# Kernel tuning notes

Hardware: AMD Instinct MI355X
Metric: run time of the kernel (lower is better)

Reference implementation:

```python
import jax, jax.numpy as jnp
import numpy as np

NEG = -1e30  # finite stand-in for -inf (keeps grads NaN-free)

T, B, V, L = 1024, 64, 128, 256


def setup_inputs() -> dict:
    key = jax.random.key(0)
    k1, k2 = jax.random.split(key)
    acts = jax.random.normal(k1, (T, B, V), dtype=jnp.float32)
    # flat concatenated labels, values in [1, V) (0 is the blank)
    labels = jax.random.randint(k2, (B * L,), 1, V, dtype=jnp.int32)
    act_lens = jnp.full((B,), T, dtype=jnp.int32)
    label_lens = jnp.full((B,), L, dtype=jnp.int32)
    return {"acts": acts, "labels": labels, "act_lens": act_lens, "label_lens": label_lens}


def _ctc_costs(acts, labels, act_lens, label_lens):
    # warp-ctc takes raw activations and applies softmax internally
    Tt, Bb, Vv = acts.shape
    Ll = labels.shape[0] // Bb
    blank = 0
    lab = labels.reshape(Bb, Ll)
    S = 2 * Ll + 1
    # extended label seq: blank, l1, blank, l2, ..., blank  -> (B, S)
    ext = jnp.full((Bb, S), blank, dtype=labels.dtype).at[:, 1::2].set(lab)
    # skip transition allowed where ext[s] != blank and ext[s] != ext[s-2]
    allow = jnp.concatenate(
        [jnp.zeros((Bb, 2), dtype=bool), (ext[:, 2:] != blank) & (ext[:, 2:] != ext[:, :-2])],
        axis=1,
    )
    log_probs = jax.nn.log_softmax(acts, axis=-1)  # (T, B, V)
    # emission log-probs along the extended label sequence: (T, B, S)
    emit_all = jnp.take_along_axis(log_probs, jnp.broadcast_to(ext[None], (Tt, Bb, S)), axis=2)

    alpha0 = (
        jnp.full((Bb, S), NEG, dtype=acts.dtype)
        .at[:, 0].set(emit_all[0, :, 0])
        .at[:, 1].set(emit_all[0, :, 1])
    )

    def step(alpha, xs):
        emit, t = xs  # emit: (B, S)
        p1 = jnp.pad(alpha[:, :-1], ((0, 0), (1, 0)), constant_values=NEG)
        p2 = jnp.pad(alpha[:, :-2], ((0, 0), (2, 0)), constant_values=NEG)
        p2 = jnp.where(allow, p2, NEG)
        m = jnp.maximum(jnp.maximum(alpha, p1), p2)
        new = m + jnp.log(jnp.exp(alpha - m) + jnp.exp(p1 - m) + jnp.exp(p2 - m)) + emit
        # freeze rows whose act_len is exhausted
        alpha = jnp.where((t < act_lens)[:, None], new, alpha)
        return alpha, None

    alphaT, _ = jax.lax.scan(step, alpha0, (emit_all[1:], jnp.arange(1, Tt)))
    end = (2 * label_lens).astype(jnp.int32)  # last blank position per example
    a_end = jnp.take_along_axis(alphaT, end[:, None], axis=1)[:, 0]
    a_end1 = jnp.take_along_axis(alphaT, (end - 1)[:, None], axis=1)[:, 0]
    return -jnp.logaddexp(a_end, a_end1)  # per-example negative log-likelihood


def reference(acts, labels, act_lens, label_lens):
    costs = _ctc_costs(acts, labels, act_lens, label_lens)
    return jnp.sum(costs)  # reduce=True, no size/length averaging
```

## Files before the change

kernel.cpp:

```cpp
#include <hip/hip_runtime.h>
#include <hip/hip_fp16.h>
#include <math.h>


#define L2E 1.4426950408889634f
#define LN2 0.6931471805599453f

constexpr int T   = 1024;
constexpr int B   = 64;
constexpr int V   = 128;
constexpr int L   = 256;
constexpr int RW  = 256;
constexpr int TP  = T + 32;

typedef float v2f __attribute__((ext_vector_type(2)));

__device__ __forceinline__ v2f pk_add(v2f a, v2f b) {
  v2f d; asm("v_pk_add_f32 %0, %1, %2" : "=v"(d) : "v"(a), "v"(b)); return d;
}
__device__ __forceinline__ v2f pk_mul(v2f a, v2f b) {
  v2f d; asm("v_pk_mul_f32 %0, %1, %2" : "=v"(d) : "v"(a), "v"(b)); return d;
}
__device__ __forceinline__ v2f pk_fma(v2f a, v2f b, v2f c) {
  v2f d; asm("v_pk_fma_f32 %0, %1, %2, %3" : "=v"(d) : "v"(a), "v"(b), "v"(c));
  return d;
}

template <int CTRL>
__device__ __forceinline__ float fdpp0(float x) {
  return __int_as_float(__builtin_amdgcn_update_dpp(
      0, __float_as_int(x), CTRL, 0xf, 0xf, true));
}
template <int CTRL>
__device__ __forceinline__ float fdppk(float x) {
  return __int_as_float(__builtin_amdgcn_update_dpp(
      __float_as_int(x), __float_as_int(x), CTRL, 0xf, 0xf, false));
}

__device__ __forceinline__ float wave_bcast63(float x) {
  return __int_as_float(__builtin_amdgcn_readlane(__float_as_int(x), 63));
}

__device__ __forceinline__ float wave_max(float x) {
  x = fmaxf(x, fdppk<0x111>(x));
  x = fmaxf(x, fdppk<0x112>(x));
  x = fmaxf(x, fdppk<0x114>(x));
  x = fmaxf(x, fdppk<0x118>(x));
  x = fmaxf(x, fdppk<0x142>(x));
  x = fmaxf(x, fdppk<0x143>(x));
  return wave_bcast63(x);
}
__device__ __forceinline__ float wave_sum_nn(float x) {
  x += fdpp0<0x111>(x);
  x += fdpp0<0x112>(x);
  x += fdpp0<0x114>(x);
  x += fdpp0<0x118>(x);
  x += fdpp0<0x142>(x);
  x += fdpp0<0x143>(x);
  return wave_bcast63(x);
}

__device__ __forceinline__ float h2f(uint bits) {
  return __half2float(__ushort_as_half((ushort)bits));
}

__global__ __launch_bounds__(512) void ctc_probs_kernel(
    const float* __restrict__ acts,
    const int* __restrict__ labels,
    ushort* __restrict__ P,
    float* __restrict__ Pbk) {
  const int w    = threadIdx.x >> 6;
  const int lane = threadIdx.x & 63;
  const int t    = blockIdx.x * 8 + w;
  const int b    = blockIdx.y;
  ushort* prow = P + ((size_t)b * TP + t) * RW;

  if (t >= T) {
    uint2 z; z.x = 0u; z.y = 0u;
    *(uint2*)(prow + 4 * lane) = z;
    if (lane == 0) {
      v2f zp; zp.x = 0.f; zp.y = 0.f;
      *(v2f*)(Pbk + ((size_t)b * TP + t) * 2) = zp;
    }
    return;
  }

  const float* row = acts + ((size_t)t * B + b) * V;
  const float2 v2 = *(const float2*)(row + 2 * lane);
  const float e0 = exp2f(fmaf(v2.x, L2E, -32.0f));
  const float e1 = exp2f(fmaf(v2.y, L2E, -32.0f));
  const float sm = wave_sum_nn(e0 + e1);
  const float r  = __builtin_amdgcn_rcpf(sm);

  const auto pk = __builtin_amdgcn_cvt_pkrtz(e0 * r, e1 * r);
  uint hp;
  __builtin_memcpy(&hp, &pk, 4);

  const int4 lv = *(const int4*)(labels + (size_t)b * L + 4 * lane);
  const uint g0 = (uint)__builtin_amdgcn_ds_bpermute((lv.x & ~1) * 2, (int)hp);
  const uint g1 = (uint)__builtin_amdgcn_ds_bpermute((lv.y & ~1) * 2, (int)hp);
  const uint g2 = (uint)__builtin_amdgcn_ds_bpermute((lv.z & ~1) * 2, (int)hp);
  const uint g3 = (uint)__builtin_amdgcn_ds_bpermute((lv.w & ~1) * 2, (int)hp);
  const uint h0 = (g0 >> ((lv.x & 1) << 4)) & 0xffffu;
  const uint h1 = (g1 >> ((lv.y & 1) << 4)) & 0xffffu;
  const uint h2 = (g2 >> ((lv.z & 1) << 4));
  const uint h3 = (g3 >> ((lv.w & 1) << 4));
  uint2 o;
  o.x = h0 | (h2 << 16);
  o.y = h1 | (h3 << 16);
  *(uint2*)(prow + 4 * lane) = o;
  if (lane == 0) {
    const float pb = e0 * r;
    v2f bp; bp.x = pb; bp.y = pb;
    *(v2f*)(Pbk + ((size_t)b * TP + t) * 2) = bp;
  }
}

__global__ __launch_bounds__(64) void ctc_dp_kernel(
    const ushort* __restrict__ P,
    const float* __restrict__ Pbk,
    const int* __restrict__ labels,
    const int* __restrict__ act_lens,
    const int* __restrict__ label_lens,
    float* __restrict__ out) {
  const int b    = blockIdx.x;
  const int lane = threadIdx.x;
  const ushort* __restrict__ Pb = P + (size_t)b * TP * RW;
  const float*  __restrict__ Bk = Pbk + (size_t)b * TP * 2;

  const int4 lv   = *(const int4*)(labels + (size_t)b * L + 4 * lane);
  const int prevw = __builtin_amdgcn_update_dpp(0, lv.w, 0x138, 0xf, 0xf, true);
  const float f0 = (lane > 0 && lv.x != 0 && lv.x != prevw) ? 1.f : 0.f;
  const float f1 = (lv.y != 0 && lv.y != lv.x) ? 1.f : 0.f;
  const float f2 = (lv.z != 0 && lv.z != lv.y) ? 1.f : 0.f;
  const float f3 = (lv.w != 0 && lv.w != lv.z) ? 1.f : 0.f;
  v2f F02; F02.x = f0; F02.y = f2;
  v2f F13; F13.x = f1; F13.y = f3;

  const int AL = act_lens[b];

  v2f P0, P1, P2, P3;
  P0.x=0.f; P0.y=0.f; P1.x=0.f; P1.y=0.f;
  P2.x=0.f; P2.y=0.f; P3.x=0.f; P3.y=0.f;
  float a8 = 0.f;
  {
    const uint2 u0 = *(const uint2*)(Pb + 4 * lane);
    const v2f bk0  = *(const v2f*)(Bk);
    const float eb0 = bk0.x;
    const float e00 = h2f(u0.x);
    if (lane == 0) { P0.x = eb0; P1.x = e00; }
  }
  int iacc = 0;
  float pend = 1.0f;

  auto step = [&](uint2 u, v2f eb) {
    const float pc = fdpp0<0x138>(P3.y);
    v2f Q; Q.x = pc; Q.y = P3.x;
    v2f E02, E13;
    E02.x = h2f(u.x); E02.y = h2f(u.x >> 16);
    E13.x = h2f(u.y); E13.y = h2f(u.y >> 16);
    const v2f S0 = pk_add(P0, Q);
    const v2f S1 = pk_add(P1, P0);
    const v2f S2 = pk_add(P2, P1);
    const v2f S3 = pk_add(P3, P2);
    const v2f T1 = pk_fma(F02, Q,  S1);
    const v2f T3 = pk_fma(F13, P1, S3);
    const float s8 = a8 + P3.y;
    P0 = pk_mul(S0, eb);
    P2 = pk_mul(S2, eb);
    P1 = pk_mul(T1, E02);
    P3 = pk_mul(T3, E13);
    a8 = s8 * eb.x;
  };

  auto measure = [&]() {
    float m = fmaxf(fmaxf(fmaxf(P0.x, P0.y), fmaxf(P1.x, P1.y)),
                    fmaxf(fmaxf(P2.x, P2.y), fmaxf(P3.x, P3.y)));
    m = fmaxf(m, a8);
    pend = wave_max(m);
  };
  auto apply = [&]() {
    const uint mb = __float_as_uint(pend);
    int e = (int)((mb >> 23) & 0xffu); if (e < 1) e = 1;
    const float r = __uint_as_float((uint)(254 - e) << 23);
    iacc += (e - 127);
    v2f rr; rr.x = r; rr.y = r;
    P0 = pk_mul(P0, rr); P1 = pk_mul(P1, rr);
    P2 = pk_mul(P2, rr); P3 = pk_mul(P3, rr);
    a8 *= r;
  };

  uint2 ev[16];
  v2f   ebk[16];
  #pragma unroll
  for (int k = 0; k < 16; ++k) {
    ev[k]  = *(const uint2*)(Pb + (size_t)(1 + k) * RW + 4 * lane);
    ebk[k] = *(const v2f*)(Bk + (size_t)(1 + k) * 2);
  }

  const ushort* pf = Pb + (size_t)17 * RW;
  const float*  bf = Bk + (size_t)17 * 2;
  int t0 = 1;
  for (int blk = 0; blk < 64; ++blk) {
    const bool fast = (t0 + 16 <= AL);
    if (fast) {
      #pragma unroll
      for (int k = 0; k < 16; ++k) {
        const uint2 u = ev[k];
        const v2f  eb = ebk[k];
        ev[k]  = *(const uint2*)(pf + (size_t)k * RW + 4 * lane);
        ebk[k] = *(const v2f*)(bf + (size_t)k * 2);
        step(u, eb);
        if (k == 3 || k == 11) measure();
        if (k == 7 || k == 15) apply();
      }
    } else {
      #pragma unroll
      for (int k = 0; k < 16; ++k) {
        const uint2 u = ev[k];
        const v2f  eb = ebk[k];
        ev[k]  = *(const uint2*)(pf + (size_t)k * RW + 4 * lane);
        ebk[k] = *(const v2f*)(bf + (size_t)k * 2);
        if ((t0 + k) < AL) step(u, eb);
        if (k == 3 || k == 11) measure();
        if (k == 7 || k == 15) apply();
      }
    }
    t0 += 16;
    pf += (size_t)16 * RW;
    bf += (size_t)16 * 2;
  }

  const int end  = 2 * label_lens[b];
  const int base = 8 * lane;
  float sel = 0.f;
  if (base     == end || base     == end - 1) sel += P0.x;
  if (base + 1 == end || base + 1 == end - 1) sel += P1.x;
  if (base + 2 == end || base + 2 == end - 1) sel += P2.x;
  if (base + 3 == end || base + 3 == end - 1) sel += P3.x;
  if (base + 4 == end || base + 4 == end - 1) sel += P0.y;
  if (base + 5 == end || base + 5 == end - 1) sel += P1.y;
  if (base + 6 == end || base + 6 == end - 1) sel += P2.y;
  if (base + 7 == end || base + 7 == end - 1) sel += P3.y;
  if (lane == 63 && (end == 512 || end - 1 == 512)) sel += a8;
  sel = wave_sum_nn(sel);
  if (lane == 0) {
    const float cost = -((log2f(sel) + (float)iacc) * LN2);
    atomicAdd(out, cost);
  }
}

extern "C" void kernel_launch(void* const* d_in, const int* in_sizes, int n_in,
                              void* d_out, int out_size, void* d_ws, size_t ws_size,
                              hipStream_t stream) {
  const float* acts       = (const float*)d_in[0];
  const int*   labels     = (const int*)d_in[1];
  const int*   act_lens   = (const int*)d_in[2];
  const int*   label_lens = (const int*)d_in[3];
  float* out = (float*)d_out;
  ushort* P   = (ushort*)d_ws;
  float*  Pbk = (float*)(P + (size_t)B * TP * RW);

  (void)hipMemsetAsync(out, 0, sizeof(float) * out_size, stream);
  ctc_probs_kernel<<<dim3(TP / 8, B), 512, 0, stream>>>(acts, labels, P, Pbk);
  ctc_dp_kernel<<<B, 64, 0, stream>>>(P, Pbk, labels, act_lens, label_lens, out);
}
```

Before: 146.9 us.

## Double-buffer DP emission loads with inline-asm global loads and explicit waitcnt

Replaces the per-step rolling register prefetch in the sequential CTC DP kernel with two 16-step register buffers. Each buffer is filled by inline-asm global loads with immediate offsets and synchronised with explicit s_waitcnt vmcnt and sched barriers. Blank probabilities are now written shifted by one step and fetched as dwordx4 pairs, and the zero-padding writes for blanks are dropped. The goal is to hide global-load latency on the latency-bound serial recurrence, at the cost of more registers and hand-managed counter correctness.

```diff
diff --git a/kernel.cpp b/kernel.cpp
--- a/kernel.cpp
+++ b/kernel.cpp
@@ -14,6 +14,8 @@
 constexpr int TP  = T + 32;
 
 typedef float v2f __attribute__((ext_vector_type(2)));
+typedef unsigned int v2u __attribute__((ext_vector_type(2)));
+typedef unsigned int v4u __attribute__((ext_vector_type(4)));
 
 __device__ __forceinline__ v2f pk_add(v2f a, v2f b) {
   v2f d; asm("v_pk_add_f32 %0, %1, %2" : "=v"(d) : "v"(a), "v"(b)); return d;
@@ -24,6 +26,17 @@
 __device__ __forceinline__ v2f pk_fma(v2f a, v2f b, v2f c) {
   v2f d; asm("v_pk_fma_f32 %0, %1, %2, %3" : "=v"(d) : "v"(a), "v"(b), "v"(c));
   return d;
+}
+
+template <int OFF>
+__device__ __forceinline__ void gload2(v2u& d, uint voff, const void* base) {
+  asm volatile("global_load_dwordx2 %0, %1, %2 offset:%3"
+               : "=v"(d) : "v"(voff), "s"(base), "i"(OFF) : "memory");
+}
+template <int OFF>
+__device__ __forceinline__ void gload4(v4u& d, uint voff, const void* base) {
+  asm volatile("global_load_dwordx4 %0, %1, %2 offset:%3"
+               : "=v"(d) : "v"(voff), "s"(base), "i"(OFF) : "memory");
 }
 
 template <int CTRL>
@@ -78,10 +91,6 @@
   if (t >= T) {
     uint2 z; z.x = 0u; z.y = 0u;
     *(uint2*)(prow + 4 * lane) = z;
-    if (lane == 0) {
-      v2f zp; zp.x = 0.f; zp.y = 0.f;
-      *(v2f*)(Pbk + ((size_t)b * TP + t) * 2) = zp;
-    }
     return;
   }
 
@@ -112,11 +121,11 @@
   if (lane == 0) {
     const float pb = e0 * r;
     v2f bp; bp.x = pb; bp.y = pb;
-    *(v2f*)(Pbk + ((size_t)b * TP + t) * 2) = bp;
-  }
-}
-
-__global__ __launch_bounds__(64) void ctc_dp_kernel(
+    *(v2f*)(Pbk + ((size_t)b * TP + t + 1) * 2) = bp;
+  }
+}
+
+__global__ __launch_bounds__(64, 1) void ctc_dp_kernel(
     const ushort* __restrict__ P,
     const float* __restrict__ Pbk,
     const int* __restrict__ labels,
@@ -144,16 +153,15 @@
   P2.x=0.f; P2.y=0.f; P3.x=0.f; P3.y=0.f;
   float a8 = 0.f;
   {
-    const uint2 u0 = *(const uint2*)(Pb + 4 * lane);
-    const v2f bk0  = *(const v2f*)(Bk);
-    const float eb0 = bk0.x;
+    const v2u u0 = *(const v2u*)(Pb + 4 * lane);
+    const float eb0 = Bk[2];
     const float e00 = h2f(u0.x);
     if (lane == 0) { P0.x = eb0; P1.x = e00; }
   }
   int iacc = 0;
   float pend = 1.0f;
 
-  auto step = [&](uint2 u, v2f eb) {
+  auto step = [&](v2u u, v2f eb) {
     const float pc = fdpp0<0x138>(P3.y);
     v2f Q; Q.x = pc; Q.y = P3.x;
     v2f E02, E13;
@@ -190,45 +198,69 @@
     a8 *= r;
   };
 
-  uint2 ev[16];
-  v2f   ebk[16];
-  #pragma unroll
-  for (int k = 0; k < 16; ++k) {
-    ev[k]  = *(const uint2*)(Pb + (size_t)(1 + k) * RW + 4 * lane);
-    ebk[k] = *(const v2f*)(Bk + (size_t)(1 + k) * 2);
-  }
-
-  const ushort* pf = Pb + (size_t)17 * RW;
-  const float*  bf = Bk + (size_t)17 * 2;
-  int t0 = 1;
-  for (int blk = 0; blk < 64; ++blk) {
-    const bool fast = (t0 + 16 <= AL);
+  v2u evA[16], evB[16];
+  v4u bbA[8],  bbB[8];
+  const uint lane8 = (uint)lane * 8u;
+
+  auto issue_blk = [&](v2u (&ev)[16], v4u (&bb)[8], int pblk) {
+    const uint pv  = (uint)((1 + 16 * pblk) * 512) + lane8;
+    const uint pv2 = pv + 4096u;
+    gload2<0>(ev[0], pv, Pb);    gload2<512>(ev[1], pv, Pb);
+    gload2<1024>(ev[2], pv, Pb); gload2<1536>(ev[3], pv, Pb);
+    gload2<2048>(ev[4], pv, Pb); gload2<2560>(ev[5], pv, Pb);
+    gload2<3072>(ev[6], pv, Pb); gload2<3584>(ev[7], pv, Pb);
+    gload2<0>(ev[8], pv2, Pb);    gload2<512>(ev[9], pv2, Pb);
+    gload2<1024>(ev[10], pv2, Pb); gload2<1536>(ev[11], pv2, Pb);
+    gload2<2048>(ev[12], pv2, Pb); gload2<2560>(ev[13], pv2, Pb);
+    gload2<3072>(ev[14], pv2, Pb); gload2<3584>(ev[15], pv2, Pb);
+    const uint bv = (uint)((2 + 16 * pblk) * 8);
+    gload4<0>(bb[0], bv, Bk);   gload4<16>(bb[1], bv, Bk);
+    gload4<32>(bb[2], bv, Bk);  gload4<48>(bb[3], bv, Bk);
+    gload4<64>(bb[4], bv, Bk);  gload4<80>(bb[5], bv, Bk);
+    gload4<96>(bb[6], bv, Bk);  gload4<112>(bb[7], bv, Bk);
+  };
+
+  auto compute_blk = [&](v2u (&ev)[16], v4u (&bb)[8], int tb, bool fast) {
     if (fast) {
       #pragma unroll
       for (int k = 0; k < 16; ++k) {
-        const uint2 u = ev[k];
-        const v2f  eb = ebk[k];
-        ev[k]  = *(const uint2*)(pf + (size_t)k * RW + 4 * lane);
-        ebk[k] = *(const v2f*)(bf + (size_t)k * 2);
-        step(u, eb);
+        const v4u q = bb[k >> 1];
+        v2f eb;
+        if (k & 1) { eb.x = __uint_as_float(q.z); eb.y = __uint_as_float(q.w); }
+        else       { eb.x = __uint_as_float(q.x); eb.y = __uint_as_float(q.y); }
+        step(ev[k], eb);
         if (k == 3 || k == 11) measure();
         if (k == 7 || k == 15) apply();
       }
     } else {
       #pragma unroll
       for (int k = 0; k < 16; ++k) {
-        const uint2 u = ev[k];
-        const v2f  eb = ebk[k];
-        ev[k]  = *(const uint2*)(pf + (size_t)k * RW + 4 * lane);
-        ebk[k] = *(const v2f*)(bf + (size_t)k * 2);
-        if ((t0 + k) < AL) step(u, eb);
+        const v4u q = bb[k >> 1];
+        v2f eb;
+        if (k & 1) { eb.x = __uint_as_float(q.z); eb.y = __uint_as_float(q.w); }
+        else       { eb.x = __uint_as_float(q.x); eb.y = __uint_as_float(q.y); }
+        if ((tb + k) < AL) step(ev[k], eb);
         if (k == 3 || k == 11) measure();
         if (k == 7 || k == 15) apply();
       }
     }
-    t0 += 16;
-    pf += (size_t)16 * RW;
-    bf += (size_t)16 * 2;
+  };
+
+  issue_blk(evA, bbA, 0);
+  issue_blk(evB, bbB, 1);
+
+  int t0 = 1;
+  #pragma unroll 1
+  for (int it = 0; it < 32; ++it) {
+    asm volatile("s_waitcnt vmcnt(24)" ::: "memory");
+    __builtin_amdgcn_sched_barrier(0);
+    compute_blk(evA, bbA, t0, (t0 + 16) <= AL);
+    { int nb = 2 * it + 2; if (nb > 63) nb = 63; issue_blk(evA, bbA, nb); }
+    asm volatile("s_waitcnt vmcnt(24)" ::: "memory");
+    __builtin_amdgcn_sched_barrier(0);
+    compute_blk(evB, bbB, t0 + 16, (t0 + 32) <= AL);
+    { int nb = 2 * it + 3; if (nb > 63) nb = 63; issue_blk(evB, bbB, nb); }
+    t0 += 32;
   }
 
   const int end  = 2 * label_lens[b];
```

After: 136.7 us. -6.9%, faster.

## Stage DP emission rows into LDS via double-buffered global_load_lds prefetch

Applied to the files above, without the earlier changes.

The serial DP kernel no longer keeps 16 rows of prefetched emissions in registers. It double-buffers 16-step blocks into LDS using direct global-to-LDS loads, waiting with explicit vmcnt and lgkmcnt counters. The blank-prob array is shifted by one row so a single 4-byte-per-lane load fetches 16 steps of blank probs, and the zero-padding write for t>=T is removed. This is meant to free VGPRs and hide global-load latency behind the recurrence. The cost is extra LDS reads on the critical path, plus a fragile hand-written waitcnt scheme and changed padding semantics.

```diff
diff --git a/kernel.cpp b/kernel.cpp
--- a/kernel.cpp
+++ b/kernel.cpp
@@ -13,7 +13,10 @@
 constexpr int RW  = 256;
 constexpr int TP  = T + 32;
 
+constexpr int LBUF = 2112;
+
 typedef float v2f __attribute__((ext_vector_type(2)));
+typedef unsigned int v2u __attribute__((ext_vector_type(2)));
 
 __device__ __forceinline__ v2f pk_add(v2f a, v2f b) {
   v2f d; asm("v_pk_add_f32 %0, %1, %2" : "=v"(d) : "v"(a), "v"(b)); return d;
@@ -24,6 +27,15 @@
 __device__ __forceinline__ v2f pk_fma(v2f a, v2f b, v2f c) {
   v2f d; asm("v_pk_fma_f32 %0, %1, %2, %3" : "=v"(d) : "v"(a), "v"(b), "v"(c));
   return d;
+}
+
+typedef __attribute__((address_space(3))) unsigned int as3_uint;
+typedef __attribute__((address_space(1))) unsigned int as1_uint;
+__device__ __forceinline__ void gl_lds16(const uint* g, uint* l) {
+  __builtin_amdgcn_global_load_lds((const as1_uint*)g, (as3_uint*)l, 16, 0, 0);
+}
+__device__ __forceinline__ void gl_lds4(const uint* g, uint* l) {
+  __builtin_amdgcn_global_load_lds((const as1_uint*)g, (as3_uint*)l, 4, 0, 0);
 }
 
 template <int CTRL>
@@ -78,10 +90,6 @@
   if (t >= T) {
     uint2 z; z.x = 0u; z.y = 0u;
     *(uint2*)(prow + 4 * lane) = z;
-    if (lane == 0) {
-      v2f zp; zp.x = 0.f; zp.y = 0.f;
-      *(v2f*)(Pbk + ((size_t)b * TP + t) * 2) = zp;
-    }
     return;
   }
 
@@ -112,17 +120,18 @@
   if (lane == 0) {
     const float pb = e0 * r;
     v2f bp; bp.x = pb; bp.y = pb;
-    *(v2f*)(Pbk + ((size_t)b * TP + t) * 2) = bp;
-  }
-}
-
-__global__ __launch_bounds__(64) void ctc_dp_kernel(
+    *(v2f*)(Pbk + ((size_t)b * TP + t + 1) * 2) = bp;
+  }
+}
+
+__global__ __launch_bounds__(64, 1) void ctc_dp_kernel(
     const ushort* __restrict__ P,
     const float* __restrict__ Pbk,
     const int* __restrict__ labels,
     const int* __restrict__ act_lens,
     const int* __restrict__ label_lens,
     float* __restrict__ out) {
+  __shared__ uint lds[2 * LBUF];
   const int b    = blockIdx.x;
   const int lane = threadIdx.x;
   const ushort* __restrict__ Pb = P + (size_t)b * TP * RW;
@@ -145,15 +154,14 @@
   float a8 = 0.f;
   {
     const uint2 u0 = *(const uint2*)(Pb + 4 * lane);
-    const v2f bk0  = *(const v2f*)(Bk);
-    const float eb0 = bk0.x;
+    const float eb0 = Bk[2];
     const float e00 = h2f(u0.x);
     if (lane == 0) { P0.x = eb0; P1.x = e00; }
   }
   int iacc = 0;
   float pend = 1.0f;
 
-  auto step = [&](uint2 u, v2f eb) {
+  auto step = [&](v2u u, v2f eb) {
     const float pc = fdpp0<0x138>(P3.y);
     v2f Q; Q.x = pc; Q.y = P3.x;
     v2f E02, E13;
@@ -190,26 +198,23 @@
     a8 *= r;
   };
 
-  uint2 ev[16];
-  v2f   ebk[16];
-  #pragma unroll
-  for (int k = 0; k < 16; ++k) {
-    ev[k]  = *(const uint2*)(Pb + (size_t)(1 + k) * RW + 4 * lane);
-    ebk[k] = *(const v2f*)(Bk + (size_t)(1 + k) * 2);
-  }
-
-  const ushort* pf = Pb + (size_t)17 * RW;
-  const float*  bf = Bk + (size_t)17 * 2;
-  int t0 = 1;
-  for (int blk = 0; blk < 64; ++blk) {
-    const bool fast = (t0 + 16 <= AL);
+  auto stage = [&](int bufi, int pblk) {
+    uint* lb = &lds[bufi * LBUF];
+    const uint* gp = (const uint*)(Pb + (size_t)(1 + 16 * pblk) * RW) + lane * 4;
+    #pragma unroll
+    for (int r2 = 0; r2 < 8; ++r2)
+      gl_lds16(gp + r2 * 256, lb + r2 * 256);
+    const uint* gb = (const uint*)(Bk + (size_t)(2 + 16 * pblk) * 2) + lane;
+    gl_lds4(gb, lb + 2048);
+  };
+
+  auto compute_blk = [&](int bufi, int tb, bool fast) {
+    const uint* lb = &lds[bufi * LBUF];
     if (fast) {
       #pragma unroll
       for (int k = 0; k < 16; ++k) {
-        const uint2 u = ev[k];
-        const v2f  eb = ebk[k];
-        ev[k]  = *(const uint2*)(pf + (size_t)k * RW + 4 * lane);
-        ebk[k] = *(const v2f*)(bf + (size_t)k * 2);
+        const v2u u = *(const v2u*)(lb + k * 128 + lane * 2);
+        const v2f eb = *(const v2f*)(lb + 2048 + 2 * k);
         step(u, eb);
         if (k == 3 || k == 11) measure();
         if (k == 7 || k == 15) apply();
@@ -217,18 +222,30 @@
     } else {
       #pragma unroll
       for (int k = 0; k < 16; ++k) {
-        const uint2 u = ev[k];
-        const v2f  eb = ebk[k];
-        ev[k]  = *(const uint2*)(pf + (size_t)k * RW + 4 * lane);
-        ebk[k] = *(const v2f*)(bf + (size_t)k * 2);
-        if ((t0 + k) < AL) step(u, eb);
+        const v2u u = *(const v2u*)(lb + k * 128 + lane * 2);
+        const v2f eb = *(const v2f*)(lb + 2048 + 2 * k);
+        if ((tb + k) < AL) step(u, eb);
         if (k == 3 || k == 11) measure();
         if (k == 7 || k == 15) apply();
       }
     }
+  };
+
+  stage(0, 0);
+  stage(1, 1);
+
+  int t0 = 1;
+  #pragma unroll 1
+  for (int it = 0; it < 64; ++it) {
+    const int cur = it & 1;
+    asm volatile("s_waitcnt vmcnt(9)" ::: "memory");
+    __builtin_amdgcn_sched_barrier(0);
+    compute_blk(cur, t0, (t0 + 16) <= AL);
+    asm volatile("s_waitcnt lgkmcnt(0)" ::: "memory");
+    __builtin_amdgcn_sched_barrier(0);
+    int nb = it + 2; if (nb > 63) nb = 63;
+    stage(cur, nb);
     t0 += 16;
-    pf += (size_t)16 * RW;
-    bf += (size_t)16 * 2;
   }
 
   const int end  = 2 * label_lens[b];
```

New measurement: 151.8 us. +3.3%, slower.
